# Performance work log

Hardware: AMD Instinct MI355X
Metric: run time of the kernel (lower is better)

Reference implementation:

```python
import jax, jax.numpy as jnp
import numpy as np

NH = 8          # attention heads
TEMP = 2.0      # gumbel temperature


def _gumbel_softmax_hard(logits, key, temperature):
    # hard=True straight-through gumbel softmax (module is in eval mode)
    g = jax.random.gumbel(key, logits.shape, logits.dtype)
    y = jax.nn.softmax((logits + g) / temperature, axis=-1)
    y_hard = jax.nn.one_hot(jnp.argmax(y, axis=-1), logits.shape[-1], dtype=y.dtype)
    return y_hard - jax.lax.stop_gradient(y) + y


def _experts(x, w1, w2, w3):
    # SwiGLU FFN over all experts at once: x [T,C], w1/w3 [E,H,C], w2 [E,C,H] -> [T,E,C]
    h = jax.nn.silu(jnp.einsum('tc,ehc->teh', x, w1)) * jnp.einsum('tc,ehc->teh', x, w3)
    return jnp.einsum('teh,ech->tec', h, w2)


def _mha(q_in, kv_in, in_w, in_b, out_w, out_b):
    C = q_in.shape[-1]
    hd = C // NH
    q = q_in @ in_w[:C].T + in_b[:C]
    k = kv_in @ in_w[C:2 * C].T + in_b[C:2 * C]
    v = kv_in @ in_w[2 * C:].T + in_b[2 * C:]
    B, Tq, _ = q.shape
    Tk = k.shape[1]
    q = q.reshape(B, Tq, NH, hd)
    k = k.reshape(B, Tk, NH, hd)
    v = v.reshape(B, Tk, NH, hd)
    scale = jnp.asarray(1.0 / np.sqrt(hd), q.dtype)
    att = jax.nn.softmax(jnp.einsum('bqhd,bkhd->bhqk', q, k) * scale, axis=-1)
    o = jnp.einsum('bhqk,bkhd->bqhd', att, v).reshape(B, Tq, C)
    return o @ out_w.T + out_b


def setup_inputs() -> dict:
    key = jax.random.key(0)
    ks = jax.random.split(key, 20)
    B, T, S, C, E, H = 2, 2048, 77, 1024, 4, 2816
    p = lambda k, sh: jax.random.normal(k, sh, jnp.float32) * 0.02
    return {
        'x': jax.random.normal(ks[0], (B, T, C), jnp.float32),
        'time': jax.random.normal(ks[1], (B,), jnp.float32),
        'caption': jax.random.normal(ks[2], (B, S, C), jnp.float32),
        'language': jax.random.randint(ks[3], (B,), 0, 9),
        'lang_embed': p(ks[4], (9, C)),
        'lang_gate_w': p(ks[5], (E, C)),
        'lang_gate_b': jnp.zeros((E,), jnp.float32),
        'lang_w1': p(ks[6], (E, H, C)),
        'lang_w2': p(ks[7], (E, C, H)),
        'lang_w3': p(ks[8], (E, H, C)),
        'in_proj_w': p(ks[9], (3 * C, C)),
        'in_proj_b': jnp.zeros((3 * C,), jnp.float32),
        'out_proj_w': p(ks[10], (C, C)),
        'out_proj_b': jnp.zeros((C,), jnp.float32),
        'cap_gate_w': p(ks[11], (E, C)),
        'cap_gate_b': jnp.zeros((E,), jnp.float32),
        'cap_w1': p(ks[12], (E, H, C)),
        'cap_w2': p(ks[13], (E, C, H)),
        'cap_w3': p(ks[14], (E, H, C)),
    }


def reference(x, time, caption, language, lang_embed, lang_gate_w, lang_gate_b,
              lang_w1, lang_w2, lang_w3, in_proj_w, in_proj_b, out_proj_w, out_proj_b,
              cap_gate_w, cap_gate_b, cap_w1, cap_w2, cap_w3):
    B, T, C = x.shape
    x_flat = x.reshape(-1, C)                                   # [B*T, C]

    # language gating (one logit vector per batch element, repeated over T tokens)
    lang_emb = lang_embed[language]                             # [B, C]
    lang_logits = lang_emb @ lang_gate_w.T + lang_gate_b        # [B, E]
    lang_probs = _gumbel_softmax_hard(lang_logits, jax.random.key(1), TEMP)
    lang_probs = jnp.repeat(lang_probs, T, axis=0)              # [B*T, E]

    lang_outputs = _experts(x_flat, lang_w1, lang_w2, lang_w3)  # [B*T, E, C]
    first_out = (lang_outputs * lang_probs[:, :, None]).sum(axis=1)  # [B*T, C]
    first_reshaped = first_out.reshape(B, T, C)

    # cross attention against caption, then per-token caption gating
    cross = _mha(first_reshaped, caption, in_proj_w, in_proj_b, out_proj_w, out_proj_b)
    cross_flat = cross.reshape(-1, C)
    cap_logits = cross_flat @ cap_gate_w.T + cap_gate_b         # [B*T, E]
    cap_probs = _gumbel_softmax_hard(cap_logits, jax.random.key(2), TEMP)

    cap_outputs = _experts(first_out, cap_w1, cap_w2, cap_w3)   # [B*T, E, C]
    second_out = (cap_outputs * cap_probs[:, :, None]).sum(axis=1)

    total_out = (first_out + second_out).reshape(B, T, C)

    all_probs = jnp.concatenate([lang_probs, cap_probs], axis=1)  # [B*T, 2E]
    expert_usage = all_probs.mean(axis=0)
    loss = (expert_usage * jnp.log(expert_usage + 1e-10)).sum()
    return total_out, loss
```

## Files before the change

### kernel.cpp

```cpp
#include <hip/hip_runtime.h>
#include <stdint.h>

#define B_ 2
#define T_ 2048
#define S_ 77
#define C_ 1024
#define E_ 4
#define H_ 2816
#define NH_ 8
#define HD_ 128
#define N_ (B_*T_)
#define MAXGB (N_/128 + E_)
#define MAXGB2 (N_/256 + E_)
#define PEsz ((size_t)H_*C_)
#define CC_ ((size_t)C_*C_)

typedef _Float16 h8 __attribute__((ext_vector_type(8)));
typedef _Float16 h4 __attribute__((ext_vector_type(4)));
typedef float f4 __attribute__((ext_vector_type(4)));

__device__ __forceinline__ void gload16(const void* g, void* l){
  __builtin_amdgcn_global_load_lds((const __attribute__((address_space(1))) void*)g,
                                   (__attribute__((address_space(3))) void*)l, 16, 0, 0);
}

__device__ __forceinline__ void xcd_swizzle_cm(int& bx, int& by){
  int nx = gridDim.x, ny = gridDim.y;
  int nwg = nx*ny;
  int wg = by*nx + bx;
  int q = nwg >> 3, r = nwg & 7;
  int xcd = wg & 7, idx = wg >> 3;
  int s = (xcd < r ? xcd*(q+1) : r*(q+1) + (xcd-r)*q) + idx;
  bx = s / ny; by = s % ny;
}

__device__ __forceinline__ uint32_t rotl32(uint32_t v, int r){ return (v<<r)|(v>>(32-r)); }
__device__ __forceinline__ void threefry2x32(uint32_t k0, uint32_t k1,
                                             uint32_t x, uint32_t y,
                                             uint32_t& o0, uint32_t& o1){
  uint32_t k2 = k0 ^ k1 ^ 0x1BD11BDAu;
  x += k0; y += k1;
#define TFR(r) { x += y; y = rotl32(y, r); y ^= x; }
  TFR(13) TFR(15) TFR(26) TFR(6)   x += k1; y += k2 + 1u;
  TFR(17) TFR(29) TFR(16) TFR(24)  x += k2; y += k0 + 2u;
  TFR(13) TFR(15) TFR(26) TFR(6)   x += k0; y += k1 + 3u;
  TFR(17) TFR(29) TFR(16) TFR(24)  x += k1; y += k2 + 4u;
  TFR(13) TFR(15) TFR(26) TFR(6)   x += k2; y += k0 + 5u;
#undef TFR
  o0 = x; o1 = y;
}
__device__ __forceinline__ float gumbel_from_bits(uint32_t bits){
  const float TINY = 1.17549435e-38f;
  float f = __uint_as_float((bits >> 9) | 0x3f800000u) - 1.0f;
  float u = fmaxf(TINY, f + TINY);
  return -logf(-logf(u));
}
__device__ __forceinline__ float jax_gumbel(uint32_t k0, uint32_t k1, uint32_t idx){
  uint32_t a, b;
  threefry2x32(k0, k1, 0u, idx, a, b);
  return gumbel_from_bits(a ^ b);
}

__device__ __forceinline__ void job_split(const float* __restrict__ s,
    _Float16* __restrict__ hi, _Float16* __restrict__ lo, long n4, int b0, int nb){
  for (long i = (long)b0*256 + threadIdx.x; i < n4; i += (long)nb*256){
    float4 v = ((const float4*)s)[i];
    h4 h, L;
    h[0]=(_Float16)v.x; h[1]=(_Float16)v.y; h[2]=(_Float16)v.z; h[3]=(_Float16)v.w;
    L[0]=(_Float16)(v.x-(float)h[0]); L[1]=(_Float16)(v.y-(float)h[1]);
    L[2]=(_Float16)(v.z-(float)h[2]); L[3]=(_Float16)(v.w-(float)h[3]);
    ((h4*)hi)[i] = h; ((h4*)lo)[i] = L;
  }
}
__device__ __forceinline__ void job_plain(const float* __restrict__ s,
    _Float16* __restrict__ d, long n4, int b0, int nb){
  for (long i = (long)b0*256 + threadIdx.x; i < n4; i += (long)nb*256){
    float4 v = ((const float4*)s)[i];
    h4 h;
    h[0]=(_Float16)v.x; h[1]=(_Float16)v.y; h[2]=(_Float16)v.z; h[3]=(_Float16)v.w;
    ((h4*)d)[i] = h;
  }
}
__device__ __forceinline__ void job_w13_plain(const float* __restrict__ w1,
    const float* __restrict__ w3, _Float16* __restrict__ dst, int nslot, int b0, int nb){
  const int K8 = C_/8;
  long total = (long)nslot * (2*H_) * K8;
  for (long i = (long)b0*256 + threadIdx.x; i < total; i += (long)nb*256){
    int kv = (int)(i & (K8-1));
    long rs = i >> 7;
    int r  = (int)(rs % (2*H_));
    int slot = (int)(rs / (2*H_));
    int gg = r >> 5, o = r & 31;
    const float* src = ((o<16)? w1 : w3) + (size_t)slot*PEsz + (size_t)(16*gg + (o&15))*C_ + kv*8;
    float4 v0 = *(const float4*)src, v1 = *(const float4*)(src+4);
    float vv[8] = {v0.x,v0.y,v0.z,v0.w,v1.x,v1.y,v1.z,v1.w};
    h8 hh;
#pragma unroll
    for (int jj=0;jj<8;++jj) hh[jj] = (_Float16)vv[jj];
    *(h8*)(dst + (size_t)slot*2*PEsz + (size_t)r*C_ + kv*8) = hh;
  }
}
__device__ __forceinline__ void job_w13_split_sel(const float* __restrict__ w1,
    const float* __restrict__ w3, int sel0, int sel1,
    _Float16* __restrict__ hi, _Float16* __restrict__ lo, int b0, int nb){
  const int K8 = C_/8;
  long total = 2L * (2*H_) * K8;
  for (long i = (long)b0*256 + threadIdx.x; i < total; i += (long)nb*256){
    int kv = (int)(i & (K8-1));
    long rs = i >> 7;
    int r  = (int)(rs % (2*H_));
    int slot = (int)(rs / (2*H_));
    int e = slot ? sel1 : sel0;
    int gg = r >> 5, o = r & 31;
    const float* src = ((o<16)? w1 : w3) + (size_t)e*PEsz + (size_t)(16*gg + (o&15))*C_ + kv*8;
    float4 v0 = *(const float4*)src, v1 = *(const float4*)(src+4);
    float vv[8] = {v0.x,v0.y,v0.z,v0.w,v1.x,v1.y,v1.z,v1.w};
    h8 hh, ll;
#pragma unroll
    for (int jj=0;jj<8;++jj){
      hh[jj] = (_Float16)vv[jj];
      ll[jj] = (_Float16)(vv[jj]-(float)hh[jj]);
    }
    size_t dof = (size_t)slot*2*PEsz + (size_t)r*C_ + kv*8;
    *(h8*)(hi + dof) = hh;
    *(h8*)(lo + dof) = ll;
  }
}
__device__ __forceinline__ void job_w2_split_sel(const float* __restrict__ w2,
    int sel0, int sel1, _Float16* __restrict__ hi, _Float16* __restrict__ lo, int b0, int nb){
  long per = (long)(PEsz/4);
  for (long i = (long)b0*256 + threadIdx.x; i < 2*per; i += (long)nb*256){
    int slot = (i >= per) ? 1 : 0;
    long ii = i - (long)slot*per;
    float4 v = ((const float4*)(w2 + (size_t)(slot?sel1:sel0)*PEsz))[ii];
    h4 h, L;
    h[0]=(_Float16)v.x; h[1]=(_Float16)v.y; h[2]=(_Float16)v.z; h[3]=(_Float16)v.w;
    L[0]=(_Float16)(v.x-(float)h[0]); L[1]=(_Float16)(v.y-(float)h[1]);
    L[2]=(_Float16)(v.z-(float)h[2]); L[3]=(_Float16)(v.w-(float)h[3]);
    ((h4*)(hi + (size_t)slot*PEsz))[ii] = h;
    ((h4*)(lo + (size_t)slot*PEsz))[ii] = L;
  }
}
__device__ __forceinline__ void job_foldw(const float* __restrict__ outw,
    const float* __restrict__ capgw, const float* __restrict__ outb,
    float* __restrict__ Wp, float* __restrict__ bp, int b0){
  int e = b0 >> 2;
  int k = ((b0 & 3) << 8) + threadIdx.x;
  const float* cg = capgw + e*C_;
  float acc = 0.f;
  for (int c = 0; c < C_; ++c) acc += cg[c] * outw[(size_t)c*C_ + k];
  Wp[e*C_ + k] = acc;
  if ((b0 & 3) == 0){
    int wv = threadIdx.x >> 6, l = threadIdx.x & 63;
    const float* cg2 = capgw + wv*C_;
    float a2 = 0.f;
    for (int c = l; c < C_; c += 64) a2 += outb[c] * cg2[c];
#pragma unroll
    for (int off = 32; off; off >>= 1) a2 += __shfl_xor(a2, off);
    if (l == 0 && e == 0) bp[wv] = a2;
  }
}

#define CVA_W13 1024
#define CVA_W2  512
#define CVA_X   256
#define CVA_TOT (CVA_W13+CVA_W2+CVA_X)
__global__ __launch_bounds__(256) void convA(
    const float* __restrict__ lang_embed, const float* __restrict__ gate_w,
    const float* __restrict__ gate_b, const int* __restrict__ language,
    const float* __restrict__ w1, const float* __restrict__ w3, const float* __restrict__ w2,
    const float* __restrict__ x,
    _Float16* __restrict__ w13hi, _Float16* __restrict__ w13lo,
    _Float16* __restrict__ w2hi, _Float16* __restrict__ w2lo,
    _Float16* __restrict__ xhi, _Float16* __restrict__ xlo,
    float* __restrict__ langP, int* __restrict__ counts)
{
  __shared__ float lds8[8];
  const int tid = threadIdx.x, w = tid>>6, l = tid&63;
  for (int p = 2*w; p < 2*w+2; ++p){
    int b = p>>2, e = p&3;
    const float* emb = lang_embed + (size_t)language[b]*C_;
    const float* gw  = gate_w + (size_t)e*C_;
    float acc = 0.f;
    for (int c = l; c < C_; c += 64) acc += emb[c]*gw[c];
#pragma unroll
    for (int off = 32; off; off >>= 1) acc += __shfl_xor(acc, off);
    if (l == 0) lds8[p] = acc + gate_b[e];
  }
  __syncthreads();
  int sel[2];
  for (int b = 0; b < 2; ++b){
    float z[4], m = -3.4e38f;
    for (int e = 0; e < 4; ++e){
      float g = jax_gumbel(0u, 1u, (uint32_t)(b*4 + e));
      z[e] = (lds8[b*4 + e] + g) * 0.5f;
      m = fmaxf(m, z[e]);
    }
    float y[4], sum = 0.f;
    for (int e = 0; e < 4; ++e){ y[e] = expf(z[e]-m); sum += y[e]; }
    for (int e = 0; e < 4; ++e) y[e] = y[e] / sum;
    int best = 0; float bv = y[0];
    for (int e = 1; e < 4; ++e) if (y[e] > bv){ bv = y[e]; best = e; }
    sel[b] = best;
    if (blockIdx.x == 0 && tid == 0){
      for (int e = 0; e < 4; ++e)
        langP[b*4 + e] = ((e == best) ? 1.0f : 0.0f) - y[e] + y[e];
    }
  }
  if (blockIdx.x == 0 && tid == 0){
    for (int e = 0; e < 4; ++e) counts[e] = 0;
  }
  int bid = blockIdx.x;
  if (bid < CVA_W13)                 job_w13_split_sel(w1, w3, sel[0], sel[1], w13hi, w13lo, bid, CVA_W13);
  else if (bid < CVA_W13+CVA_W2)     job_w2_split_sel(w2, sel[0], sel[1], w2hi, w2lo, bid-CVA_W13, CVA_W2);
  else                               job_split(x, xhi, xlo, (long)((size_t)N_*C_/4), bid-CVA_W13-CVA_W2, CVA_X);
}

__global__ __launch_bounds__(512,2) void gemm_gate_split(
    const _Float16* __restrict__ Ahi, const _Float16* __restrict__ Alo,
    const _Float16* __restrict__ Bhi, const _Float16* __restrict__ Blo,
    _Float16* __restrict__ Hhi, _Float16* __restrict__ Hlo)
{
  __shared__ __align__(16) char smem[147456];
  const int tid = threadIdx.x, w = tid>>6, l = tid&63;
  const int lm = l&15, g = l>>4;
  const int wm = w>>1, wn = w&1;
  int bx = blockIdx.x, by = blockIdx.y;
  xcd_swizzle_cm(bx, by);
  const int n0 = bx<<7;
  const int m0 = by<<8;
  const size_t eoff = (m0 >= T_) ? (size_t)2*PEsz : 0;

  const _Float16* srcA[4]; const _Float16* srcB[2];
#pragma unroll
  for (int jj=0;jj<4;++jj){
    int c = jj*512 + tid, r = c>>3, s = c&7;
    int st = s ^ (r&7);
    srcA[jj] = (st<4 ? Ahi : Alo) + (size_t)(m0 + r)*C_ + ((st&3)<<3);
  }
#pragma unroll
  for (int jj=0;jj<2;++jj){
    int c = jj*512 + tid, r = c>>3, s = c&7;
    int st = s ^ (r&7);
    srcB[jj] = (st<4 ? Bhi : Blo) + eoff + (size_t)(n0 + r)*C_ + ((st&3)<<3);
  }

#define STG(ts, bi) { \
    int k0 = (ts)<<5; \
    char* db = smem + (bi)*49152; \
    _Pragma("unroll") \
    for (int jj=0;jj<4;++jj) gload16(srcA[jj]+k0, db + (jj*512 + w*64)*16); \
    _Pragma("unroll") \
    for (int jj=0;jj<2;++jj) gload16(srcB[jj]+k0, db + 32768 + (jj*512 + w*64)*16); \
  }

  const int shi = (g ^ (lm&7)) << 4;
  int aoff[4], boff[4];
#pragma unroll
  for (int i=0;i<4;++i){
    aoff[i] = ((wm*64 + i*16 + lm)<<7) + shi;
    boff[i] = 32768 + ((wn*64 + i*16 + lm)<<7) + shi;
  }

  f4 acc[4][4] = {};
  const int nt = C_/32;
  STG(0,0) STG(1,1)
  for (int t=0; t<nt; ++t){
    const int bi = t%3;
    const int ts = (t+2 < nt) ? t+2 : 0;
    STG(ts, (t+2)%3)
    asm volatile("s_waitcnt vmcnt(12)" ::: "memory");
    __builtin_amdgcn_s_barrier();
    asm volatile("" ::: "memory");
    const char* base = smem + bi*49152;
    h8 ah[4], bh[4];
#pragma unroll
    for (int i=0;i<4;++i){ ah[i] = *(const h8*)(base + aoff[i]); bh[i] = *(const h8*)(base + boff[i]); }
    __builtin_amdgcn_s_setprio(1);
#pragma unroll
    for (int mi=0;mi<4;++mi)
#pragma unroll
      for (int ni=0;ni<4;++ni)
        acc[mi][ni] = __builtin_amdgcn_mfma_f32_16x16x32_f16(ah[mi], bh[ni], acc[mi][ni],0,0,0);
    __builtin_amdgcn_s_setprio(0);
    h8 bl[4];
#pragma unroll
    for (int i=0;i<4;++i) bl[i] = *(const h8*)(base + (boff[i]^64));
    __builtin_amdgcn_s_setprio(1);
#pragma unroll
    for (int mi=0;mi<4;++mi)
#pragma unroll
      for (int ni=0;ni<4;++ni)
        acc[mi][ni] = __builtin_amdgcn_mfma_f32_16x16x32_f16(ah[mi], bl[ni], acc[mi][ni],0,0,0);
    __builtin_amdgcn_s_setprio(0);
    h8 al[4];
#pragma unroll
    for (int i=0;i<4;++i) al[i] = *(const h8*)(base + (aoff[i]^64));
    __builtin_amdgcn_s_setprio(1);
#pragma unroll
    for (int mi=0;mi<4;++mi)
#pragma unroll
      for (int ni=0;ni<4;++ni)
        acc[mi][ni] = __builtin_amdgcn_mfma_f32_16x16x32_f16(al[mi], bh[ni], acc[mi][ni],0,0,0);
    __builtin_amdgcn_s_setprio(0);
    asm volatile("" ::: "memory");
    __builtin_amdgcn_s_barrier();
  }
#undef STG

#pragma unroll
  for (int mi=0;mi<4;++mi){
#pragma unroll
    for (int p=0;p<2;++p){
      int hc = ((n0 + wn*64)>>1) + p*16 + lm;
#pragma unroll
      for (int j=0;j<4;++j){
        int rl = wm*64 + mi*16 + (g<<2) + j;
        float s1 = acc[mi][2*p][j], s3 = acc[mi][2*p+1][j];
        float hval = s1/(1.f+expf(-s1))*s3;
        size_t row = (size_t)(m0 + rl);
        _Float16 hh = (_Float16)hval;
        Hhi[row*H_ + hc] = hh;
        Hlo[row*H_ + hc] = (_Float16)(hval - (float)hh);
      }
    }
  }
}

__global__ __launch_bounds__(512,2) void gemm_gate_plain(
    const _Float16* __restrict__ A, const _Float16* __restrict__ Bw,
    _Float16* __restrict__ Hout,
    const int* __restrict__ bmap_e, const int* __restrict__ bmap_s,
    const int* __restrict__ offs, const int* __restrict__ perm)
{
  __shared__ __align__(16) char smem[147456];
  const int tid = threadIdx.x, w = tid>>6, l = tid&63;
  const int lm = l&15, g = l>>4;
  const int wm = w>>1, wn = w&1;
  int bx = blockIdx.x, by = blockIdx.y;
  xcd_swizzle_cm(bx, by);
  const int e = bmap_e[by]; if (e<0) return;
  const int m0 = bmap_s[by];
  int v = offs[e+1]-m0; const int valid = v>256?256:v;
  const size_t eoff = (size_t)e*2*PEsz;
  const int n0 = bx<<7;

  const _Float16* srcA[4]; const _Float16* srcB[2];
#pragma unroll
  for (int jj=0;jj<4;++jj){
    int c = jj*512 + tid, r = c>>3, s = c&7;
    int st = s ^ (r&7);
    int ia = m0 + r; ia = (ia<N_) ? ia : (N_-1);
    srcA[jj] = A + (size_t)perm[ia]*C_ + (st<<3);
  }
#pragma unroll
  for (int jj=0;jj<2;++jj){
    int c = jj*512 + tid, r = c>>3, s = c&7;
    int st = s ^ (r&7);
    srcB[jj] = Bw + eoff + (size_t)(n0 + r)*C_ + (st<<3);
  }

#define STG(ts, bi) { \
    int k0 = (ts)<<6; \
    char* db = smem + (bi)*49152; \
    _Pragma("unroll") \
    for (int jj=0;jj<4;++jj) gload16(srcA[jj]+k0, db + (jj*512 + w*64)*16); \
    _Pragma("unroll") \
    for (int jj=0;jj<2;++jj) gload16(srcB[jj]+k0, db + 32768 + (jj*512 + w*64)*16); \
  }

  const int shi = (g ^ (lm&7)) << 4;
  int aoff[4], boff[4];
#pragma unroll
  for (int i=0;i<4;++i){
    aoff[i] = ((wm*64 + i*16 + lm)<<7) + shi;
    boff[i] = 32768 + ((wn*64 + i*16 + lm)<<7) + shi;
  }

  f4 acc[4][4] = {};
  const int nt = C_/64;
  STG(0,0) STG(1,1)
  for (int t=0; t<nt; ++t){
    const int bi = t%3;
    const int ts = (t+2 < nt) ? t+2 : 0;
    STG(ts, (t+2)%3)
    asm volatile("s_waitcnt vmcnt(12)" ::: "memory");
    __builtin_amdgcn_s_barrier();
    asm volatile("" ::: "memory");
    const char* base = smem + bi*49152;
#pragma unroll
    for (int kk=0;kk<2;++kk){
      h8 af[4], bf[4];
      const int x = kk<<6;
#pragma unroll
      for (int i=0;i<4;++i){ af[i] = *(const h8*)(base + (aoff[i]^x)); bf[i] = *(const h8*)(base + (boff[i]^x)); }
      __builtin_amdgcn_s_setprio(1);
#pragma unroll
      for (int mi=0;mi<4;++mi)
#pragma unroll
        for (int ni=0;ni<4;++ni)
          acc[mi][ni] = __builtin_amdgcn_mfma_f32_16x16x32_f16(af[mi], bf[ni], acc[mi][ni],0,0,0);
      __builtin_amdgcn_s_setprio(0);
    }
    asm volatile("" ::: "memory");
    __builtin_amdgcn_s_barrier();
  }
#undef STG

#pragma unroll
  for (int mi=0;mi<4;++mi){
#pragma unroll
    for (int p=0;p<2;++p){
      int hc = ((n0 + wn*64)>>1) + p*16 + lm;
#pragma unroll
      for (int j=0;j<4;++j){
        int rl = wm*64 + mi*16 + (g<<2) + j;
        if (rl >= valid) continue;
        float s1 = acc[mi][2*p][j], s3 = acc[mi][2*p+1][j];
        Hout[(size_t)(m0 + rl)*H_ + hc] = (_Float16)(s1/(1.f+expf(-s1))*s3);
      }
    }
  }
}

template<int EPI, int NSEG, int EXPM>
__device__ __forceinline__ void gemm8_body(
    char* smem,
    const _Float16* __restrict__ A0, const _Float16* __restrict__ A1,
    const _Float16* __restrict__ B0, const _Float16* __restrict__ B1,
    const float* __restrict__ bias, float* __restrict__ Cf32,
    _Float16* __restrict__ O0, _Float16* __restrict__ O1,
    const int* __restrict__ bmap_e, const int* __restrict__ bmap_s,
    const int* __restrict__ offs, const int* __restrict__ perm,
    int M, int K, int Nw, size_t bstride_e, int bx, int by)
{
  const int tid = threadIdx.x, w = tid>>6, l = tid&63;
  const int lm = l&15, g = l>>4;
  const int wm = w>>1, wn = w&1;
  const int n0 = bx<<7;
  int m0, valid = 128; size_t eoff = 0;
  if constexpr (EXPM==3){
    int e = bmap_e[by]; if (e<0) return;
    m0 = bmap_s[by];
    int v = offs[e+1]-m0; valid = v>128?128:v;
    eoff = (size_t)e*bstride_e;
  } else {
    m0 = by<<7;
    if constexpr (EXPM==1) eoff = (m0>=T_) ? bstride_e : 0;
  }
  const int cAe = (((tid&7) ^ ((tid>>3)&7)) << 3);
  size_t rbA[4], rbB[4];
#pragma unroll
  for (int j=0;j<4;++j){
    int r = (j<<5) + (tid>>3);
    int ia = m0 + r;
    if constexpr (EXPM==3){ ia = (ia < N_) ? ia : (N_-1); }
    else { if (ia > M-1) ia = M-1; }
    rbA[j] = (size_t)ia*K + cAe;
    rbB[j] = eoff + (size_t)(n0+r)*K + cAe;
  }
  const int tps = K>>6, nt = NSEG*tps;

#define STAGE8(tt, cc) { \
    int sg = 0; \
    if constexpr (NSEG==3){ sg = ((tt)>=2*tps) ? 2 : (((tt)>=tps)?1:0); } \
    const _Float16* Asrc = (sg==1) ? A1 : A0; \
    const _Float16* Bsrc = (sg==2) ? B1 : B0; \
    int kk0 = ((tt) - sg*tps)<<6; \
    char* db = smem + (cc)*32768 + w*1024; \
    _Pragma("unroll") \
    for (int j=0;j<4;++j) gload16(Asrc + rbA[j] + kk0, db + j*4096); \
    _Pragma("unroll") \
    for (int j=0;j<4;++j) gload16(Bsrc + rbB[j] + kk0, db + 16384 + j*4096); \
  }

  int aoff[2][4], boff[2][4];
#pragma unroll
  for (int kk=0;kk<2;++kk){
#pragma unroll
    for (int i=0;i<4;++i){
      int ra = wm*64 + i*16 + lm;
      aoff[kk][i] = (ra<<7) + (((kk<<6)+(g<<4)) ^ ((ra&7)<<4));
      int rb = wn*64 + i*16 + lm;
      boff[kk][i] = (rb<<7) + (((kk<<6)+(g<<4)) ^ ((rb&7)<<4));
    }
  }

  f4 acc[4][4] = {};
  STAGE8(0, 0)
  for (int t=0; t<nt; ++t){
    const int c = t&1;
    if (t+1 < nt){
      STAGE8(t+1, c^1)
      asm volatile("s_waitcnt vmcnt(8)" ::: "memory");
    } else {
      asm volatile("s_waitcnt vmcnt(0)" ::: "memory");
    }
    __builtin_amdgcn_s_barrier();
    const char* Ab = smem + c*32768;
    const char* Bb = Ab + 16384;
#pragma unroll
    for (int kk=0;kk<2;++kk){
      h8 af[4], bf[4];
#pragma unroll
      for (int i=0;i<4;++i){
        af[i] = *(const h8*)(Ab + aoff[kk][i]);
        bf[i] = *(const h8*)(Bb + boff[kk][i]);
      }
      __builtin_amdgcn_s_setprio(1);
#pragma unroll
      for (int mi=0;mi<4;++mi)
#pragma unroll
        for (int ni=0;ni<4;++ni)
          acc[mi][ni] = __builtin_amdgcn_mfma_f32_16x16x32_f16(af[mi], bf[ni], acc[mi][ni],0,0,0);
      __builtin_amdgcn_s_setprio(0);
      __builtin_amdgcn_s_barrier();
    }
  }

#pragma unroll
  for (int mi=0;mi<4;++mi){
    const int rl0 = wm*64 + mi*16 + (g<<2);
#pragma unroll
    for (int ni=0;ni<4;++ni){
      int col = n0 + wn*64 + ni*16 + lm;
#pragma unroll
      for (int j=0;j<4;++j){
        int rl = rl0 + j;
        float vv = acc[mi][ni][j];
        if constexpr (EPI==1){
          int grow = m0 + rl;
          if (grow < M){
            float vb = vv + (bias ? bias[col] : 0.f);
            _Float16 hh = (_Float16)vb;
            O0[(size_t)grow*Nw + col] = hh;
            O1[(size_t)grow*Nw + col] = (_Float16)(vb - (float)hh);
          }
        } else {
          if (rl < valid){
            int orig = perm[m0 + rl];
            size_t o = (size_t)orig*C_ + col;
            Cf32[o] = (float)O0[o] + (float)O1[o] + vv;
          }
        }
      }
    }
  }
#undef STAGE8
}

template<int EPI, int NSEG, int EXPM>
__global__ __launch_bounds__(256,2) void gemm8(
    const _Float16* __restrict__ A0, const _Float16* __restrict__ A1,
    const _Float16* __restrict__ B0, const _Float16* __restrict__ B1,
    const float* __restrict__ bias, float* __restrict__ Cf32,
    _Float16* __restrict__ O0, _Float16* __restrict__ O1,
    const int* __restrict__ bmap_e, const int* __restrict__ bmap_s,
    const int* __restrict__ offs, const int* __restrict__ perm,
    int M, int K, int Nw, size_t bstride_e)
{
  __shared__ __align__(16) char smem[65536];
  int bx = blockIdx.x, by = blockIdx.y;
  xcd_swizzle_cm(bx, by);
  gemm8_body<EPI,NSEG,EXPM>(smem, A0,A1,B0,B1,bias,Cf32,O0,O1,
                            bmap_e,bmap_s,offs,perm,M,K,Nw,bstride_e,bx,by);
}

__global__ __launch_bounds__(256,2) void ffn1_out_fused(
    const _Float16* __restrict__ Hbh, const _Float16* __restrict__ Hbl,
    const _Float16* __restrict__ w2hi, const _Float16* __restrict__ w2lo,
    _Float16* __restrict__ Fh, _Float16* __restrict__ Fl,
    const float* __restrict__ in_w,
    const float* __restrict__ cap_w1, const float* __restrict__ cap_w3,
    const float* __restrict__ caption,
    _Float16* __restrict__ inwh, _Float16* __restrict__ inwl,
    _Float16* __restrict__ capw13,
    _Float16* __restrict__ caph, _Float16* __restrict__ capl)
{
  __shared__ __align__(16) char smem[65536];
  int id = blockIdx.x;
  if (id < 256){
    gemm8_body<1,3,1>(smem, Hbh, Hbl, w2hi, w2lo, nullptr, nullptr, Fh, Fl,
                      nullptr,nullptr,nullptr,nullptr, N_, H_, C_, PEsz, id&7, id>>3);
  } else {
    int cid = id - 256;
    if (cid < 352)      job_w13_plain(cap_w1, cap_w3, capw13, 4, cid, 352);
    else if (cid < 496) job_split(in_w, inwh, inwl, (long)(3*CC_/4), cid-352, 144);
    else                job_split(caption, caph, capl, (long)((size_t)B_*S_*C_/4), cid-496, 16);
  }
}

__global__ __launch_bounds__(256,2) void gemm_qkv(
    const _Float16* __restrict__ Fh, const _Float16* __restrict__ Fl,
    const _Float16* __restrict__ caph, const _Float16* __restrict__ capl,
    const _Float16* __restrict__ inwh, const _Float16* __restrict__ inwl,
    const float* __restrict__ in_b,
    _Float16* __restrict__ Qh, _Float16* __restrict__ Ql,
    _Float16* __restrict__ KVh, _Float16* __restrict__ KVl,
    const float* __restrict__ out_w, const float* __restrict__ cap_gw,
    const float* __restrict__ out_b, float* __restrict__ Wp, float* __restrict__ bp)
{
  __shared__ __align__(16) char smem[65536];
  int id = blockIdx.x;
  if (id < 256){
    gemm8_body<1,3,0>(smem, Fh, Fl, inwh, inwl, in_b, nullptr, Qh, Ql,
                      nullptr,nullptr,nullptr,nullptr, N_, C_, C_, 0, id&7, id>>3);
  } else if (id < 288){
    int cid = id - 256;
    gemm8_body<1,3,0>(smem, caph, capl, inwh + CC_, inwl + CC_, in_b + C_,
                      nullptr, KVh, KVl, nullptr,nullptr,nullptr,nullptr,
                      B_*S_, C_, 2*C_, 0, cid & 15, cid >> 4);
  } else {
    job_foldw(out_w, cap_gw, out_b, Wp, bp, id-288);
  }
}

#define SP5 5
#define KSTR 136
#define VSTR 104
__global__ __launch_bounds__(256) void attn_fused(
    const _Float16* __restrict__ Qh, const _Float16* __restrict__ Ql,
    const _Float16* __restrict__ KVh, const _Float16* __restrict__ KVl,
    _Float16* __restrict__ AOh, _Float16* __restrict__ AOl,
    const float* __restrict__ cap_w2, _Float16* __restrict__ capw2f)
{
  __shared__ __align__(16) _Float16 Usm[2*128*VSTR];
  __shared__ __align__(16) _Float16 Psm[2*64*VSTR];
  int id = blockIdx.x;
  if (id >= 512){ job_plain(cap_w2, capw2f, (long)(4*PEsz/4), id-512, 128); return; }
  _Float16* Kh_s = Usm;
  _Float16* Kl_s = Usm + 128*VSTR;
  _Float16* VTh  = Usm;
  _Float16* VTl  = Usm + 128*VSTR;
  _Float16* Ph   = Psm;
  _Float16* Pl   = Psm + 64*VSTR;

  const int tid = threadIdx.x;
  const int w = tid>>6, l = tid&63, lm = l&15, g = l>>4;
  const int b = id >> 8, h = (id >> 5) & 7, q0 = (id & 31) << 6;
  const float scale = 0.08838834764831845f;

  for (int i = tid; i < 64*VSTR; i += 256) ((uint32_t*)Psm)[i] = 0;
  {
    int oct = tid & 15, s0 = tid >> 4;
    for (int s = s0; s < 80; s += 16){
      h8 vh = {}, vl = {};
      if (s < S_){
        size_t ga = ((size_t)(b*S_ + s))*(2*C_) + h*HD_ + oct*8;
        vh = *(const h8*)(KVh + ga);
        vl = *(const h8*)(KVl + ga);
      }
      *(h8*)(Kh_s + s*KSTR + oct*8) = vh;
      *(h8*)(Kl_s + s*KSTR + oct*8) = vl;
    }
  }
  h8 qh[4], ql[4];
  {
    size_t qrow = (size_t)(b*T_ + q0 + w*16 + lm);
    const _Float16* qph = Qh + qrow*C_ + h*HD_ + g*8;
    const _Float16* qpl = Ql + qrow*C_ + h*HD_ + g*8;
#pragma unroll
    for (int ks=0; ks<4; ++ks){ qh[ks] = *(const h8*)(qph + ks*32); ql[ks] = *(const h8*)(qpl + ks*32); }
  }
  __syncthreads();

  f4 sc[SP5] = {};
#pragma unroll
  for (int ks=0; ks<4; ++ks){
#pragma unroll
    for (int nt=0; nt<SP5; ++nt){
      h8 kh = *(const h8*)(Kh_s + (nt*16+lm)*KSTR + ks*32 + g*8);
      h8 kl = *(const h8*)(Kl_s + (nt*16+lm)*KSTR + ks*32 + g*8);
      sc[nt] = __builtin_amdgcn_mfma_f32_16x16x32_f16(qh[ks], kh, sc[nt],0,0,0);
      sc[nt] = __builtin_amdgcn_mfma_f32_16x16x32_f16(ql[ks], kh, sc[nt],0,0,0);
      sc[nt] = __builtin_amdgcn_mfma_f32_16x16x32_f16(qh[ks], kl, sc[nt],0,0,0);
    }
  }

  float mx[4] = {-3e38f,-3e38f,-3e38f,-3e38f};
#pragma unroll
  for (int nt=0; nt<SP5; ++nt){
    bool valid = (nt*16+lm) < S_;
#pragma unroll
    for (int j=0;j<4;++j){
      float v = valid ? sc[nt][j]*scale : -3e38f;
      sc[nt][j] = v;
      mx[j] = fmaxf(mx[j], v);
    }
  }
#pragma unroll
  for (int off=1; off<16; off<<=1){
#pragma unroll
    for (int j=0;j<4;++j) mx[j] = fmaxf(mx[j], __shfl_xor(mx[j], off));
  }
  float sm[4] = {0,0,0,0};
#pragma unroll
  for (int nt=0; nt<SP5; ++nt){
    bool valid = (nt*16+lm) < S_;
#pragma unroll
    for (int j=0;j<4;++j){
      float p = valid ? expf(sc[nt][j]-mx[j]) : 0.f;
      sc[nt][j] = p; sm[j] += p;
    }
  }
#pragma unroll
  for (int off=1; off<16; off<<=1){
#pragma unroll
    for (int j=0;j<4;++j) sm[j] += __shfl_xor(sm[j], off);
  }
#pragma unroll
  for (int nt=0; nt<SP5; ++nt){
#pragma unroll
    for (int j=0;j<4;++j){
      int col = nt*16 + lm;
      if (col < S_){
        float p = sc[nt][j] / sm[j];
        int row = w*16 + g*4 + j;
        _Float16 ph = (_Float16)p;
        Ph[row*VSTR + col] = ph;
        Pl[row*VSTR + col] = (_Float16)(p - (float)ph);
      }
    }
  }
  __syncthreads();

  for (int i = tid; i < 128*VSTR; i += 256) ((uint32_t*)Usm)[i] = 0;
  __syncthreads();
  {
    int oct = tid & 15, s0 = tid >> 4;
    for (int s = s0; s < S_; s += 16){
      size_t ga = ((size_t)(b*S_ + s))*(2*C_) + C_ + h*HD_ + oct*8;
      h8 vh = *(const h8*)(KVh + ga);
      h8 vl = *(const h8*)(KVl + ga);
#pragma unroll
      for (int i2=0;i2<8;++i2){
        VTh[(oct*8+i2)*VSTR + s] = vh[i2];
        VTl[(oct*8+i2)*VSTR + s] = vl[i2];
      }
    }
  }
  __syncthreads();

  h8 pah[3], pal[3];
#pragma unroll
  for (int ks=0;ks<3;++ks){
    pah[ks] = *(const h8*)(Ph + (w*16+lm)*VSTR + ks*32 + g*8);
    pal[ks] = *(const h8*)(Pl + (w*16+lm)*VSTR + ks*32 + g*8);
  }
#pragma unroll
  for (int nt=0; nt<8; ++nt){
    f4 o = {};
#pragma unroll
    for (int ks=0;ks<3;++ks){
      h8 vh = *(const h8*)(VTh + (nt*16+lm)*VSTR + ks*32 + g*8);
      h8 vl = *(const h8*)(VTl + (nt*16+lm)*VSTR + ks*32 + g*8);
      o = __builtin_amdgcn_mfma_f32_16x16x32_f16(pah[ks], vh, o,0,0,0);
      o = __builtin_amdgcn_mfma_f32_16x16x32_f16(pal[ks], vh, o,0,0,0);
      o = __builtin_amdgcn_mfma_f32_16x16x32_f16(pah[ks], vl, o,0,0,0);
    }
#pragma unroll
    for (int j=0;j<4;++j){
      size_t orow = (size_t)(b*T_ + q0 + w*16 + g*4 + j);
      size_t oa = orow*C_ + h*HD_ + nt*16 + lm;
      _Float16 hh = (_Float16)o[j];
      AOh[oa] = hh;
      AOl[oa] = (_Float16)(o[j] - (float)hh);
    }
  }
}

__global__ __launch_bounds__(256) void cap_gate(
    const _Float16* __restrict__ AOh, const _Float16* __restrict__ AOl,
    const float* __restrict__ Wp, const float* __restrict__ bp,
    const float* __restrict__ gb,
    int* __restrict__ cap_sel, float* __restrict__ capP, int* __restrict__ counts)
{
  int tid = threadIdx.x, wave = tid >> 6, lane = tid & 63;
  for (int r = 0; r < 2; ++r){
    int row = (blockIdx.x << 3) + (wave << 1) + r;
    float av[16];
#pragma unroll
    for (int i = 0; i < 16; ++i){
      int c = lane + (i << 6);
      av[i] = (float)AOh[(size_t)row*C_ + c] + (float)AOl[(size_t)row*C_ + c];
    }
    float lg[E_];
#pragma unroll
    for (int e = 0; e < E_; ++e){
      const float* wv = Wp + (size_t)e * C_;
      float p = 0.f;
#pragma unroll
      for (int i = 0; i < 16; ++i) p += av[i] * wv[lane + (i << 6)];
#pragma unroll
      for (int off = 32; off; off >>= 1) p += __shfl_xor(p, off);
      lg[e] = p + bp[e] + gb[e];
    }
    if (lane == 0){
      float z[E_], m = -3.4e38f;
      for (int e = 0; e < E_; ++e){
        float gmb = jax_gumbel(0u, 2u, (uint32_t)(row*E_ + e));
        z[e] = (lg[e] + gmb) * 0.5f;
        m = fmaxf(m, z[e]);
      }
      float y[E_], sum = 0.f;
      for (int e = 0; e < E_; ++e){ y[e] = expf(z[e] - m); sum += y[e]; }
      for (int e = 0; e < E_; ++e) y[e] = y[e] / sum;
      int best = 0; float bv = y[0];
      for (int e = 1; e < E_; ++e) if (y[e] > bv){ bv = y[e]; best = e; }
      cap_sel[row] = best;
      atomicAdd(&counts[best], 1);
      for (int e = 0; e < E_; ++e)
        capP[(size_t)row*E_ + e] = ((e == best) ? 1.0f : 0.0f) - y[e] + y[e];
    }
  }
}

__global__ __launch_bounds__(256) void finalize(
    const int* __restrict__ counts, const int* __restrict__ cap_sel,
    int* __restrict__ offs,
    int* __restrict__ bmap_e, int* __restrict__ bmap_s,
    int* __restrict__ bmap_e2, int* __restrict__ bmap_s2,
    int* __restrict__ perm,
    const float* __restrict__ capP, const float* __restrict__ langP,
    float* __restrict__ out_loss)
{
  __shared__ int loffs[5];
  __shared__ int lcur[4];
  __shared__ float red[4][256];
  int tid = threadIdx.x;
  if (blockIdx.x == 0){
    if (tid == 0){
      loffs[0] = 0;
      for (int e = 0; e < E_; ++e){ loffs[e+1] = loffs[e] + counts[e]; lcur[e] = loffs[e]; }
      for (int e = 0; e < E_+1; ++e) offs[e] = loffs[e];
      int idx = 0;
      for (int e = 0; e < E_; ++e)
        for (int s = loffs[e]; s < loffs[e+1]; s += 128){ bmap_e[idx] = e; bmap_s[idx] = s; ++idx; }
      for (; idx < MAXGB; ++idx) bmap_e[idx] = -1;
      int idx2 = 0;
      for (int e = 0; e < E_; ++e)
        for (int s = loffs[e]; s < loffs[e+1]; s += 256){ bmap_e2[idx2] = e; bmap_s2[idx2] = s; ++idx2; }
      for (; idx2 < MAXGB2; ++idx2) bmap_e2[idx2] = -1;
    }
    __syncthreads();
    for (int row = tid; row < N_; row += 256){
      int e = cap_sel[row];
      int pos = atomicAdd(&lcur[e], 1);
      perm[pos] = row;
    }
  } else {
    float p0=0.f, p1=0.f, p2=0.f, p3=0.f;
    for (int r = tid; r < N_; r += 256){
      const float* p = capP + (size_t)r*E_;
      p0 += p[0]; p1 += p[1]; p2 += p[2]; p3 += p[3];
    }
    red[0][tid]=p0; red[1][tid]=p1; red[2][tid]=p2; red[3][tid]=p3;
    __syncthreads();
    for (int s = 128; s > 0; s >>= 1){
      if (tid < s){
        red[0][tid]+=red[0][tid+s]; red[1][tid]+=red[1][tid+s];
        red[2][tid]+=red[2][tid+s]; red[3][tid]+=red[3][tid+s];
      }
      __syncthreads();
    }
    if (tid == 0){
      float loss = 0.f;
      for (int e = 0; e < E_; ++e){
        float ul = (langP[e] + langP[E_ + e]) * 0.5f;
        loss += ul * logf(ul + 1e-10f);
      }
      for (int e = 0; e < E_; ++e){
        float uc = red[e][0] * (1.0f / N_);
        loss += uc * logf(uc + 1e-10f);
      }
      out_loss[0] = loss;
    }
  }
}

extern "C" void kernel_launch(void* const* d_in, const int* in_sizes, int n_in,
                              void* d_out, int out_size, void* d_ws, size_t ws_size,
                              hipStream_t stream)
{
  const float* x          = (const float*)d_in[0];
  const float* caption    = (const float*)d_in[2];
  const int*   language   = (const int*)  d_in[3];
  const float* lang_embed = (const float*)d_in[4];
  const float* lang_gw    = (const float*)d_in[5];
  const float* lang_gb    = (const float*)d_in[6];
  const float* lang_w1    = (const float*)d_in[7];
  const float* lang_w2    = (const float*)d_in[8];
  const float* lang_w3    = (const float*)d_in[9];
  const float* in_w       = (const float*)d_in[10];
  const float* in_b       = (const float*)d_in[11];
  const float* out_w      = (const float*)d_in[12];
  const float* out_b      = (const float*)d_in[13];
  const float* cap_gw     = (const float*)d_in[14];
  const float* cap_gb     = (const float*)d_in[15];
  const float* cap_w1     = (const float*)d_in[16];
  const float* cap_w2     = (const float*)d_in[17];
  const float* cap_w3     = (const float*)d_in[18];
  float* out = (float*)d_out;

  const size_t NC = (size_t)N_*C_;
  const size_t NHe = (size_t)N_*H_;
  const size_t KVel = (size_t)B_*S_*2*C_;
  const size_t CAPel = (size_t)B_*S_*C_;

  char* base = (char*)d_ws;
  size_t cur = 0;
  auto alloc = [&](size_t bytes)->char*{
    char* p = base + cur;
    cur += (bytes + 255) & ~(size_t)255;
    return p;
  };
  _Float16* Qh = (_Float16*)alloc(NC*2);
  _Float16* Ql = (_Float16*)alloc(NC*2);
  char* kvreg = alloc(KVel*4);
  _Float16* KVh = (_Float16*)kvreg;
  _Float16* KVl = KVh + KVel;
  float* capP   = (float*)alloc((size_t)N_*E_*4);
  float* langP  = (float*)alloc(64);
  float* Wp     = (float*)alloc(E_*C_*4);
  float* bp     = (float*)alloc(64);
  int* cap_sel  = (int*)alloc(N_*4);
  int* counts   = (int*)alloc(64);
  int* offs     = (int*)alloc(64);
  int* bmap_e   = (int*)alloc(MAXGB*4);
  int* bmap_s   = (int*)alloc(MAXGB*4);
  int* bmap_e2  = (int*)alloc(MAXGB2*4);
  int* bmap_s2  = (int*)alloc(MAXGB2*4);
  int* perm     = (int*)alloc(N_*4);
  _Float16* xAO_hi = (_Float16*)alloc(NC*2);
  _Float16* xAO_lo = (_Float16*)alloc(NC*2);
  _Float16* cap_hi = (_Float16*)alloc(CAPel*2);
  _Float16* cap_lo = (_Float16*)alloc(CAPel*2);
  _Float16* Hb_hi  = (_Float16*)alloc(NHe*2);
  _Float16* Hb_lo  = (_Float16*)alloc(NHe*2);
  _Float16* F_hi   = (_Float16*)alloc(NC*2);
  _Float16* F_lo   = (_Float16*)alloc(NC*2);
  _Float16* Wreg = (_Float16*)alloc(2*( (size_t)3*CC_*2 + CC_*2 + 3*4*PEsz ));
  _Float16* w13hi = Wreg;
  _Float16* w13lo = Wreg + 4*PEsz;
  _Float16* w2hi  = Wreg + 8*PEsz;
  _Float16* w2lo  = Wreg + 10*PEsz;
  _Float16* capw13f = Wreg;
  _Float16* capw2f  = Wreg + 8*PEsz;
  _Float16* inw_hi  = Wreg + 12*PEsz;
  _Float16* inw_lo  = inw_hi + 3*CC_;

  convA<<<CVA_TOT, 256, 0, stream>>>(
      lang_embed, lang_gw, lang_gb, language,
      lang_w1, lang_w3, lang_w2, x,
      w13hi, w13lo, w2hi, w2lo, xAO_hi, xAO_lo, langP, counts);

  gemm_gate_split<<<dim3((2*H_)/128, N_/256), 512, 0, stream>>>(
      xAO_hi, xAO_lo, w13hi, w13lo, Hb_hi, Hb_lo);

  ffn1_out_fused<<<768, 256, 0, stream>>>(
      Hb_hi, Hb_lo, w2hi, w2lo, F_hi, F_lo,
      in_w, cap_w1, cap_w3, caption,
      inw_hi, inw_lo, capw13f, cap_hi, cap_lo);

  gemm_qkv<<<304, 256, 0, stream>>>(
      F_hi, F_lo, cap_hi, cap_lo, inw_hi, inw_lo, in_b,
      Qh, Ql, KVh, KVl, out_w, cap_gw, out_b, Wp, bp);

  attn_fused<<<640, 256, 0, stream>>>(Qh, Ql, KVh, KVl, xAO_hi, xAO_lo, cap_w2, capw2f);

  cap_gate<<<N_/8, 256, 0, stream>>>(xAO_hi, xAO_lo, Wp, bp, cap_gb, cap_sel, capP, counts);

  finalize<<<2, 256, 0, stream>>>(counts, cap_sel, offs, bmap_e, bmap_s,
                                  bmap_e2, bmap_s2, perm, capP, langP, out + NC);

  _Float16* H2 = Hb_hi;
  gemm_gate_plain<<<dim3((2*H_)/128, MAXGB2), 512, 0, stream>>>(
      F_hi, capw13f, H2, bmap_e2, bmap_s2, offs, perm);

  gemm8<2,1,3><<<dim3(C_/128, MAXGB), 256, 0, stream>>>(
      H2, nullptr, capw2f, nullptr, nullptr, out, F_hi, F_lo,
      bmap_e, bmap_s, offs, perm, N_, H_, C_, PEsz);
}
```

Before: 660.1 us.

## Interleave next-stage global-to-LDS loads with MFMA phases and drop trailing barrier

In both expert GEMM kernels, the block load of the tile two stages ahead is split into small groups of global_load_lds calls. These groups are spread between the MFMA sub-phases instead of being issued in one burst at the top of the loop. The end-of-iteration barrier is removed, relying on the single top-of-loop barrier to protect the triple-buffered slot being overwritten. Wait counts are tightened to vmcnt(6), or vmcnt(0) on the last step, and the dummy wrap-around loads at the tail are skipped. The aim is to hide memory issue latency behind matrix math and cut one barrier per K step, at the cost of a more fragile ordering between the vmcnt arithmetic and buffer reuse.

```diff
diff --git a/kernel.cpp b/kernel.cpp
--- a/kernel.cpp
+++ b/kernel.cpp
@@ -245,7 +245,7 @@
     srcB[jj] = (st<4 ? Bhi : Blo) + eoff + (size_t)(n0 + r)*C_ + ((st&3)<<3);
   }
 
-#define STG(ts, bi) { \
+#define STGF(ts, bi) { \
     int k0 = (ts)<<5; \
     char* db = smem + (bi)*49152; \
     _Pragma("unroll") \
@@ -264,15 +264,21 @@
 
   f4 acc[4][4] = {};
   const int nt = C_/32;
-  STG(0,0) STG(1,1)
+  STGF(0,0) STGF(1,1)
   for (int t=0; t<nt; ++t){
     const int bi = t%3;
-    const int ts = (t+2 < nt) ? t+2 : 0;
-    STG(ts, (t+2)%3)
-    asm volatile("s_waitcnt vmcnt(12)" ::: "memory");
+    const bool ds = (t+2 < nt);
+    const int k2 = (t+2)<<5;
+    char* db2 = smem + ((t+2)%3)*49152;
+    if (t+1 < nt) { asm volatile("s_waitcnt vmcnt(6)" ::: "memory"); }
+    else          { asm volatile("s_waitcnt vmcnt(0)" ::: "memory"); }
     __builtin_amdgcn_s_barrier();
     asm volatile("" ::: "memory");
     const char* base = smem + bi*49152;
+    if (ds){
+      gload16(srcA[0]+k2, db2 + (0*512 + w*64)*16);
+      gload16(srcA[1]+k2, db2 + (1*512 + w*64)*16);
+    }
     h8 ah[4], bh[4];
 #pragma unroll
     for (int i=0;i<4;++i){ ah[i] = *(const h8*)(base + aoff[i]); bh[i] = *(const h8*)(base + boff[i]); }
@@ -283,6 +289,10 @@
       for (int ni=0;ni<4;++ni)
         acc[mi][ni] = __builtin_amdgcn_mfma_f32_16x16x32_f16(ah[mi], bh[ni], acc[mi][ni],0,0,0);
     __builtin_amdgcn_s_setprio(0);
+    if (ds){
+      gload16(srcA[2]+k2, db2 + (2*512 + w*64)*16);
+      gload16(srcA[3]+k2, db2 + (3*512 + w*64)*16);
+    }
     h8 bl[4];
 #pragma unroll
     for (int i=0;i<4;++i) bl[i] = *(const h8*)(base + (boff[i]^64));
@@ -293,6 +303,10 @@
       for (int ni=0;ni<4;++ni)
         acc[mi][ni] = __builtin_amdgcn_mfma_f32_16x16x32_f16(ah[mi], bl[ni], acc[mi][ni],0,0,0);
     __builtin_amdgcn_s_setprio(0);
+    if (ds){
+      gload16(srcB[0]+k2, db2 + 32768 + (0*512 + w*64)*16);
+      gload16(srcB[1]+k2, db2 + 32768 + (1*512 + w*64)*16);
+    }
     h8 al[4];
 #pragma unroll
     for (int i=0;i<4;++i) al[i] = *(const h8*)(base + (aoff[i]^64));
@@ -304,9 +318,8 @@
         acc[mi][ni] = __builtin_amdgcn_mfma_f32_16x16x32_f16(al[mi], bh[ni], acc[mi][ni],0,0,0);
     __builtin_amdgcn_s_setprio(0);
     asm volatile("" ::: "memory");
-    __builtin_amdgcn_s_barrier();
-  }
-#undef STG
+  }
+#undef STGF
 
 #pragma unroll
   for (int mi=0;mi<4;++mi){
@@ -360,7 +373,7 @@
     srcB[jj] = Bw + eoff + (size_t)(n0 + r)*C_ + (st<<3);
   }
 
-#define STG(ts, bi) { \
+#define STGF(ts, bi) { \
     int k0 = (ts)<<6; \
     char* db = smem + (bi)*49152; \
     _Pragma("unroll") \
@@ -379,17 +392,30 @@
 
   f4 acc[4][4] = {};
   const int nt = C_/64;
-  STG(0,0) STG(1,1)
+  STGF(0,0) STGF(1,1)
   for (int t=0; t<nt; ++t){
     const int bi = t%3;
-    const int ts = (t+2 < nt) ? t+2 : 0;
-    STG(ts, (t+2)%3)
-    asm volatile("s_waitcnt vmcnt(12)" ::: "memory");
+    const bool ds = (t+2 < nt);
+    const int k2 = (t+2)<<6;
+    char* db2 = smem + ((t+2)%3)*49152;
+    if (t+1 < nt) { asm volatile("s_waitcnt vmcnt(6)" ::: "memory"); }
+    else          { asm volatile("s_waitcnt vmcnt(0)" ::: "memory"); }
     __builtin_amdgcn_s_barrier();
     asm volatile("" ::: "memory");
     const char* base = smem + bi*49152;
 #pragma unroll
     for (int kk=0;kk<2;++kk){
+      if (ds){
+        if (kk == 0){
+          gload16(srcA[0]+k2, db2 + (0*512 + w*64)*16);
+          gload16(srcA[1]+k2, db2 + (1*512 + w*64)*16);
+          gload16(srcA[2]+k2, db2 + (2*512 + w*64)*16);
+        } else {
+          gload16(srcA[3]+k2, db2 + (3*512 + w*64)*16);
+          gload16(srcB[0]+k2, db2 + 32768 + (0*512 + w*64)*16);
+          gload16(srcB[1]+k2, db2 + 32768 + (1*512 + w*64)*16);
+        }
+      }
       h8 af[4], bf[4];
       const int x = kk<<6;
 #pragma unroll
@@ -403,9 +429,8 @@
       __builtin_amdgcn_s_setprio(0);
     }
     asm volatile("" ::: "memory");
-    __builtin_amdgcn_s_barrier();
-  }
-#undef STG
+  }
+#undef STGF
 
 #pragma unroll
   for (int mi=0;mi<4;++mi){
```

Result: faster. 640.0 us (-3.1%).
